# Kernel tuning notes

Hardware: AMD Instinct MI355X
Metric: run time of the kernel (lower is better)

The kernel has to match this reference:

```python
import jax, jax.numpy as jnp
import numpy as np

LOW_THRESH, HIGH_THRESH = 0.1, 0.2   # kornia canny defaults
HYST_ITERS = 10                      # fixed-point hysteresis iterations (fixed for jit)


def _gaussian_kernel5(sigma=1.0):
    x = jnp.arange(5, dtype=jnp.float32) - 2.0
    g = jnp.exp(-0.5 * (x / sigma) ** 2)
    g = g / g.sum()
    return jnp.outer(g, g)  # [5,5]


def _conv2d(x, k):
    # x: [B,1,H,W]; k: [kh,kw]; reflect pad + VALID conv == SAME with reflect border
    kh, kw = k.shape
    xp = jnp.pad(x, ((0, 0), (0, 0), (kh // 2, kh // 2), (kw // 2, kw // 2)), mode="reflect")
    return jax.lax.conv_general_dilated(
        xp, k[None, None], (1, 1), "VALID",
        dimension_numbers=("NCHW", "OIHW", "NCHW"))


def _shift(x, dy, dx):
    # value of neighbor at (i+dy, j+dx), zero-padded border; x: [B,1,H,W]
    H, W = x.shape[2], x.shape[3]
    xp = jnp.pad(x, ((0, 0), (0, 0), (1, 1), (1, 1)))
    return xp[:, :, 1 + dy:1 + dy + H, 1 + dx:1 + dx + W]


def _canny_edges(img):
    # img: [B,3,H,W] in [0,1] -> binary edge map [B,1,H,W]
    gray = 0.299 * img[:, :1] + 0.587 * img[:, 1:2] + 0.114 * img[:, 2:3]
    blur = _conv2d(gray, _gaussian_kernel5())
    sobel_x = jnp.array([[-1., 0., 1.], [-2., 0., 2.], [-1., 0., 1.]], jnp.float32)
    gx = _conv2d(blur, sobel_x)
    gy = _conv2d(blur, sobel_x.T)
    mag = jnp.sqrt(gx * gx + gy * gy + 1e-12)
    ang = jnp.arctan2(gy, gx)

    # non-maximum suppression: quantize gradient direction to 4 bins (0/45/90/135 deg)
    b = jnp.mod(jnp.round(ang / (jnp.pi / 4.0)), 4).astype(jnp.int32)  # [B,1,H,W]
    n_pos = jnp.stack([_shift(mag, 0, 1), _shift(mag, 1, 1),
                       _shift(mag, 1, 0), _shift(mag, 1, -1)], axis=0)  # [4,B,1,H,W]
    n_neg = jnp.stack([_shift(mag, 0, -1), _shift(mag, -1, -1),
                       _shift(mag, -1, 0), _shift(mag, -1, 1)], axis=0)
    n1 = jnp.take_along_axis(n_pos, b[None], axis=0)[0]
    n2 = jnp.take_along_axis(n_neg, b[None], axis=0)[0]
    nms = jnp.where((mag >= n1) & (mag >= n2), mag, 0.0)

    # double threshold: strong=1.0, weak=0.5
    edges = jnp.where(nms >= HIGH_THRESH, 1.0,
                      jnp.where(nms >= LOW_THRESH, 0.5, 0.0))

    # hysteresis: weak pixels with a strong 8-neighbor become strong (iterated)
    def body(_, e):
        strong = (e == 1.0).astype(e.dtype)
        nb = jax.lax.reduce_window(strong, 0.0, jax.lax.max,
                                   (1, 1, 3, 3), (1, 1, 1, 1), "SAME")
        promoted = (e == 0.5) & (nb > 0.5)
        return jnp.where(promoted, 1.0, e)

    edges = jax.lax.fori_loop(0, HYST_ITERS, body, edges)
    return (edges == 1.0).astype(jnp.float32)


def setup_inputs() -> dict:
    key = jax.random.key(0)
    k1, k2 = jax.random.split(key)
    shape = (16, 3, 512, 512)
    return {"y_hat": jax.random.uniform(k1, shape, jnp.float32),
            "y": jax.random.uniform(k2, shape, jnp.float32)}


def reference(y_hat, y):
    y_hat_edges = _canny_edges(y_hat)
    y_edges = _canny_edges(y)
    return jnp.mean(jnp.abs(y_hat_edges - y_edges))  # F.l1_loss, mean reduction
```

## Files before the change

### kernel.cpp

```cpp
#include <hip/hip_runtime.h>
#include <math.h>

#define H 512
#define W 512
#define IMG (H*W)
#define NIMG 32
#define NSTRIP 10
#define SW 56
#define RB 32
#define NBAND 16

typedef unsigned long long u64;

__device__ __forceinline__ int reflect_idx(int i, int n) {
    if (i < 0) i = -i;
    if (i >= n) i = 2 * n - 2 - i;
    return i;
}

__device__ __forceinline__ float bperm_f(int addr, float v) {
    return __int_as_float(__builtin_amdgcn_ds_bpermute(addr, __float_as_int(v)));
}

#define S0 0.05448868454964294f
#define S1 0.35317871110251920f
#define S2 0.94551131545035710f
#define S3 1.29364257779496160f
#define A1 0.05448868454964294f
#define A2 0.24420134200323332f
#define A3 0.34813126234460456f

__global__ __launch_bounds__(256, 5) void k_edges(const float* __restrict__ yhat,
                                                  const float* __restrict__ yy,
                                                  u64* __restrict__ strongP,
                                                  u64* __restrict__ weakP) {
    const int wid = blockIdx.x * 4 + (threadIdx.x >> 6);
    const int lane = threadIdx.x & 63;
    const int n = wid / (NSTRIP * NBAND);
    const int rem = wid - n * (NSTRIP * NBAND);
    const int s = rem / NBAND;
    const int band = rem - s * NBAND;
    const int y0 = band * RB;
    const float* src = (n < 16) ? (yhat + (size_t)n * 3 * IMG)
                                : (yy + (size_t)(n - 16) * 3 * IMG);

    const int c = s * SW - 4 + lane;
    const int cx = reflect_idx(c, W);
    const bool colok = ((unsigned)c < (unsigned)W);
    const u64 omask = (s == 9) ? 0xFFull : 0x00FFFFFFFFFFFFFFull;

    const int aM3 = ((lane - 3) << 2), aM2 = ((lane - 2) << 2), aM1 = ((lane - 1) << 2);
    const int aP1 = ((lane + 1) << 2), aP2 = ((lane + 2) << 2), aP3 = ((lane + 3) << 2);

    float hx[7], hy[7];
#pragma unroll
    for (int j = 0; j < 7; j++) { hx[j] = 0.f; hy[j] = 0.f; }

    const u64 outBase = ((size_t)n * NSTRIP + s) * H;

    float r0, g0c, b0, r1, g1c, b1;
    {
        const float* p0 = src + (size_t)reflect_idx(y0 - 4, H) * W + cx;
        const float* p1 = src + (size_t)reflect_idx(y0 - 3, H) * W + cx;
        r0 = p0[0]; g0c = p0[IMG]; b0 = p0[2 * IMG];
        r1 = p1[0]; g1c = p1[IMG]; b1 = p1[2 * IMG];
    }

#define PREFETCH(k)                                                             \
    {                                                                           \
        const float* p0 = src + (size_t)reflect_idx(y0 - 4 + 2 * (k), H) * W + cx; \
        const float* p1 = src + (size_t)reflect_idx(y0 - 3 + 2 * (k), H) * W + cx; \
        r0 = p0[0]; g0c = p0[IMG]; b0 = p0[2 * IMG];                            \
        r1 = p1[0]; g1c = p1[IMG]; b1 = p1[2 * IMG];                            \
    }

#define HPUSH(gv)                                                               \
    {                                                                           \
        float gm1 = bperm_f(aM1, gv), gp1 = bperm_f(aP1, gv);                   \
        float gm2 = bperm_f(aM2, gv), gp2 = bperm_f(aP2, gv);                   \
        float gm3 = bperm_f(aM3, gv), gp3 = bperm_f(aP3, gv);                   \
        _Pragma("unroll")                                                       \
        for (int j = 0; j < 6; j++) { hx[j] = hx[j + 1]; hy[j] = hy[j + 1]; }   \
        hx[6] = A3 * (gp1 - gm1) + A2 * (gp2 - gm2) + A1 * (gp3 - gm3);         \
        hy[6] = S3 * gv + S2 * (gp1 + gm1) + S1 * (gp2 + gm2) + S0 * (gp3 + gm3); \
    }

#define MAG(mr, mv, mvL, mvR, dv)                                               \
    {                                                                           \
        float gx = S3 * hx[3] + S2 * (hx[4] + hx[2])                            \
                 + S1 * (hx[5] + hx[1]) + S0 * (hx[6] + hx[0]);                 \
        float gy = A3 * (hy[4] - hy[2]) + A2 * (hy[5] - hy[1])                  \
                 + A1 * (hy[6] - hy[0]);                                        \
        bool okm = colok && ((unsigned)(mr) < (unsigned)H);                     \
        mv = okm ? (gx * gx + gy * gy + 1e-12f) : 0.f;                          \
        mvL = bperm_f(aM1, mv);                                                 \
        mvR = bperm_f(aP1, mv);                                                 \
        float ax = fabsf(gx), ay = fabsf(gy);                                   \
        dv = (ay <= 0.4142135623730951f * ax) ? 0                               \
           : (ay >= 2.414213562373095f * ax) ? 2                                \
           : (((gx > 0.f) == (gy > 0.f)) ? 1 : 3);                              \
    }

#pragma unroll
    for (int k = 0; k < 3; k++) {
        float ga = 0.299f * r0 + 0.587f * g0c + 0.114f * b0;
        float gb = 0.299f * r1 + 0.587f * g1c + 0.114f * b1;
        PREFETCH(k + 1);
        HPUSH(ga);
        HPUSH(gb);
    }

    float mm1, mm1L, mm1R, m0, m0L, m0R;
    int dir0;
    {
        float ga = 0.299f * r0 + 0.587f * g0c + 0.114f * b0;
        float gb = 0.299f * r1 + 0.587f * g1c + 0.114f * b1;
        PREFETCH(4);
        int dtmp;
        HPUSH(ga);
        MAG(y0 - 1, mm1, mm1L, mm1R, dtmp);
        (void)dtmp;
        HPUSH(gb);
        MAG(y0, m0, m0L, m0R, dir0);
    }

#pragma unroll 4
    for (int k = 4; k < 20; k++) {
        float ga = 0.299f * r0 + 0.587f * g0c + 0.114f * b0;
        float gb = 0.299f * r1 + 0.587f * g1c + 0.114f * b1;
        if (k < 19) PREFETCH(k + 1);

        float ma, maL, maR, mb, mbL, mbR;
        int da, db;
        HPUSH(ga);
        MAG(y0 + 2 * k - 7, ma, maL, maR, da);
        HPUSH(gb);
        MAG(y0 + 2 * k - 6, mb, mbL, mbR, db);

        float n1 = (dir0 == 0) ? m0R : (dir0 == 1) ? maR : (dir0 == 2) ? ma : maL;
        float n2 = (dir0 == 0) ? m0L : (dir0 == 1) ? mm1L : (dir0 == 2) ? mm1 : mm1R;
        bool ok0 = (m0 >= n1) && (m0 >= n2);
        u64 bs0 = __ballot(ok0 && (m0 >= 0.04f));
        u64 bw0 = __ballot(ok0 && (m0 >= 0.01f));

        float n3 = (da == 0) ? maR : (da == 1) ? mbR : (da == 2) ? mb : mbL;
        float n4 = (da == 0) ? maL : (da == 1) ? m0L : (da == 2) ? m0 : m0R;
        bool ok1 = (ma >= n3) && (ma >= n4);
        u64 bs1 = __ballot(ok1 && (ma >= 0.04f));
        u64 bw1 = __ballot(ok1 && (ma >= 0.01f));

        if (lane == 0) {
            int t0 = y0 + 2 * k - 8;
            ulonglong2 vs, vw;
            vs.x = (bs0 >> 4) & omask; vs.y = (bs1 >> 4) & omask;
            vw.x = (bw0 >> 4) & omask; vw.y = (bw1 >> 4) & omask;
            *(ulonglong2*)&strongP[outBase + t0] = vs;
            *(ulonglong2*)&weakP[outBase + t0] = vw;
        }

        mm1 = ma; mm1L = maL; mm1R = maR;
        m0 = mb; m0L = mbL; m0R = mbR;
        dir0 = db;
    }
#undef PREFETCH
#undef HPUSH
#undef MAG
}

__device__ __forceinline__ u64 ldw10(const u64* p, int img, int y, int q, bool ok) {
    return (ok && q >= 0 && q < NSTRIP) ? p[((size_t)img * NSTRIP + q) * H + y] : 0ULL;
}

__global__ __launch_bounds__(256) void k_hyst(const u64* __restrict__ strongP,
                                              const u64* __restrict__ weakP,
                                              unsigned int* __restrict__ partials) {
    __shared__ unsigned int part[4];
    const int wy = threadIdx.x >> 6;
    const int wave = blockIdx.x * 4 + wy;
    const int lane = threadIdx.x & 63;
    const int tile = wave & 255;
    const int pair = wave >> 8;
    const int tx0 = (tile & 15) * 32;
    const int ty0 = (tile >> 4) * 32;

    const int y = ty0 - 10 + lane;
    const bool rowok = (lane < 52) && (y >= 0) && (y < H);
    const int yc = rowok ? y : 0;

    const int x = tx0 - 10;
    const int q0 = (x < 0) ? -1 : (x / 56);
    const int r = x - 56 * q0;
    const int sh1 = 56 - r;
    const bool need3 = (r > 48);
    const int sh2 = 112 - r;

    const int imgA = pair, imgB = pair + 16;
    u64 sA, wA, sB, wB;
    {
        u64 w0, w1, w2;
        w0 = ldw10(strongP, imgA, yc, q0, rowok);
        w1 = ldw10(strongP, imgA, yc, q0 + 1, rowok);
        w2 = need3 ? ldw10(strongP, imgA, yc, q0 + 2, rowok) : 0ULL;
        sA = (w0 >> r) | (w1 << sh1) | (need3 ? (w2 << sh2) : 0ULL);
        w0 = ldw10(weakP, imgA, yc, q0, rowok);
        w1 = ldw10(weakP, imgA, yc, q0 + 1, rowok);
        w2 = need3 ? ldw10(weakP, imgA, yc, q0 + 2, rowok) : 0ULL;
        wA = (w0 >> r) | (w1 << sh1) | (need3 ? (w2 << sh2) : 0ULL);
        w0 = ldw10(strongP, imgB, yc, q0, rowok);
        w1 = ldw10(strongP, imgB, yc, q0 + 1, rowok);
        w2 = need3 ? ldw10(strongP, imgB, yc, q0 + 2, rowok) : 0ULL;
        sB = (w0 >> r) | (w1 << sh1) | (need3 ? (w2 << sh2) : 0ULL);
        w0 = ldw10(weakP, imgB, yc, q0, rowok);
        w1 = ldw10(weakP, imgB, yc, q0 + 1, rowok);
        w2 = need3 ? ldw10(weakP, imgB, yc, q0 + 2, rowok) : 0ULL;
        wB = (w0 >> r) | (w1 << sh1) | (need3 ? (w2 << sh2) : 0ULL);
    }

#pragma unroll
    for (int it = 0; it < 10; it++) {
        u64 up = __shfl_up(sA, 1), dn = __shfl_down(sA, 1);
        u64 t = up | sA | dn;
        sA |= (t | (t << 1) | (t >> 1)) & wA;
        up = __shfl_up(sB, 1); dn = __shfl_down(sB, 1);
        t = up | sB | dn;
        sB |= (t | (t << 1) | (t >> 1)) & wB;
    }

    unsigned int cgt = 0;
    if (lane >= 10 && lane < 42) {
        const u64 mask = ((1ULL << 42) - (1ULL << 10));
        cgt = (unsigned int)__popcll((sA ^ sB) & mask);
    }
#pragma unroll
    for (int off = 32; off > 0; off >>= 1) cgt += __shfl_down(cgt, off);
    if (lane == 0) part[wy] = cgt;
    __syncthreads();
    if (threadIdx.x == 0)
        partials[blockIdx.x] = part[0] + part[1] + part[2] + part[3];
}

__global__ __launch_bounds__(256) void k_final(const unsigned int* __restrict__ partials,
                                               float* __restrict__ out) {
    __shared__ unsigned int part[4];
    unsigned int c = 0;
    for (int i = threadIdx.x; i < 1024; i += 256) c += partials[i];
#pragma unroll
    for (int off = 32; off > 0; off >>= 1) c += __shfl_down(c, off);
    const int lane = threadIdx.x & 63;
    const int wy = threadIdx.x >> 6;
    if (lane == 0) part[wy] = c;
    __syncthreads();
    if (threadIdx.x == 0)
        out[0] = (float)(part[0] + part[1] + part[2] + part[3]) * (1.0f / 4194304.0f);
}

extern "C" void kernel_launch(void* const* d_in, const int* in_sizes, int n_in,
                              void* d_out, int out_size, void* d_ws, size_t ws_size,
                              hipStream_t stream) {
    const float* yhat = (const float*)d_in[0];
    const float* yy = (const float*)d_in[1];

    u64* strongP = (u64*)d_ws;
    u64* weakP = strongP + (size_t)NIMG * NSTRIP * H;
    unsigned int* partials = (unsigned int*)(weakP + (size_t)NIMG * NSTRIP * H);

    k_edges<<<1280, 256, 0, stream>>>(yhat, yy, strongP, weakP);

    k_hyst<<<1024, 256, 0, stream>>>(strongP, weakP, partials);
    k_final<<<1, 256, 0, stream>>>(partials, (float*)d_out);
}
```

Before: 135.0 us.

## Halve edge row bands, raise occupancy, and fold final reduction into atomics

Each edge-detection wave now covers 16-row bands instead of 32, which doubles the grid and raises the occupancy hint from 5 to 8 so more waves are in flight to hide latency. The cost is more recomputed halo rows per band. The separate one-block final-reduction kernel is dropped. Hysteresis blocks now add their counts atomically, and the last block to finish writes the mean. Counters are zeroed inside the edge kernel, which removes one launch but relies on that kernel finishing before the hysteresis kernel starts.

```diff
diff --git a/kernel.cpp b/kernel.cpp
--- a/kernel.cpp
+++ b/kernel.cpp
@@ -7,8 +7,10 @@
 #define NIMG 32
 #define NSTRIP 10
 #define SW 56
-#define RB 32
-#define NBAND 16
+#define RB 16
+#define NBAND 32
+#define NPAIR (RB/2)
+#define NHYST_BLK 1024
 
 typedef unsigned long long u64;
 
@@ -30,12 +32,16 @@
 #define A2 0.24420134200323332f
 #define A3 0.34813126234460456f
 
-__global__ __launch_bounds__(256, 5) void k_edges(const float* __restrict__ yhat,
+__global__ __launch_bounds__(256, 8) void k_edges(const float* __restrict__ yhat,
                                                   const float* __restrict__ yy,
                                                   u64* __restrict__ strongP,
-                                                  u64* __restrict__ weakP) {
+                                                  u64* __restrict__ weakP,
+                                                  unsigned int* __restrict__ counters) {
     const int wid = blockIdx.x * 4 + (threadIdx.x >> 6);
     const int lane = threadIdx.x & 63;
+
+    if (wid == 0 && lane == 0) { counters[0] = 0u; counters[1] = 0u; }
+
     const int n = wid / (NSTRIP * NBAND);
     const int rem = wid - n * (NSTRIP * NBAND);
     const int s = rem / NBAND;
@@ -125,10 +131,10 @@
     }
 
 #pragma unroll 4
-    for (int k = 4; k < 20; k++) {
+    for (int k = 4; k < 4 + NPAIR; k++) {
         float ga = 0.299f * r0 + 0.587f * g0c + 0.114f * b0;
         float gb = 0.299f * r1 + 0.587f * g1c + 0.114f * b1;
-        if (k < 19) PREFETCH(k + 1);
+        if (k < 3 + NPAIR) PREFETCH(k + 1);
 
         float ma, maL, maR, mb, mbL, mbR;
         int da, db;
@@ -173,7 +179,8 @@
 
 __global__ __launch_bounds__(256) void k_hyst(const u64* __restrict__ strongP,
                                               const u64* __restrict__ weakP,
-                                              unsigned int* __restrict__ partials) {
+                                              unsigned int* __restrict__ counters,
+                                              float* __restrict__ out) {
     __shared__ unsigned int part[4];
     const int wy = threadIdx.x >> 6;
     const int wave = blockIdx.x * 4 + wy;
@@ -235,23 +242,16 @@
     for (int off = 32; off > 0; off >>= 1) cgt += __shfl_down(cgt, off);
     if (lane == 0) part[wy] = cgt;
     __syncthreads();
-    if (threadIdx.x == 0)
-        partials[blockIdx.x] = part[0] + part[1] + part[2] + part[3];
-}
-
-__global__ __launch_bounds__(256) void k_final(const unsigned int* __restrict__ partials,
-                                               float* __restrict__ out) {
-    __shared__ unsigned int part[4];
-    unsigned int c = 0;
-    for (int i = threadIdx.x; i < 1024; i += 256) c += partials[i];
-#pragma unroll
-    for (int off = 32; off > 0; off >>= 1) c += __shfl_down(c, off);
-    const int lane = threadIdx.x & 63;
-    const int wy = threadIdx.x >> 6;
-    if (lane == 0) part[wy] = c;
-    __syncthreads();
-    if (threadIdx.x == 0)
-        out[0] = (float)(part[0] + part[1] + part[2] + part[3]) * (1.0f / 4194304.0f);
+    if (threadIdx.x == 0) {
+        unsigned int tot = part[0] + part[1] + part[2] + part[3];
+        atomicAdd(&counters[0], tot);
+        __threadfence();
+        unsigned int t = atomicAdd(&counters[1], 1u);
+        if (t == NHYST_BLK - 1) {
+            unsigned int total = atomicAdd(&counters[0], 0u);
+            out[0] = (float)total * (1.0f / 4194304.0f);
+        }
+    }
 }
 
 extern "C" void kernel_launch(void* const* d_in, const int* in_sizes, int n_in,
@@ -262,10 +262,9 @@
 
     u64* strongP = (u64*)d_ws;
     u64* weakP = strongP + (size_t)NIMG * NSTRIP * H;
-    unsigned int* partials = (unsigned int*)(weakP + (size_t)NIMG * NSTRIP * H);
-
-    k_edges<<<1280, 256, 0, stream>>>(yhat, yy, strongP, weakP);
-
-    k_hyst<<<1024, 256, 0, stream>>>(strongP, weakP, partials);
-    k_final<<<1, 256, 0, stream>>>(partials, (float*)d_out);
-}
+    unsigned int* counters = (unsigned int*)(weakP + (size_t)NIMG * NSTRIP * H);
+
+    k_edges<<<2560, 256, 0, stream>>>(yhat, yy, strongP, weakP, counters);
+
+    k_hyst<<<1024, 256, 0, stream>>>(strongP, weakP, counters, (float*)d_out);
+}
```

Measured after the change: 181.0 us. +34.0%, slower.
